# Performance work log

Measured on AMD Instinct MI355X. Metric: run time of the kernel, lower is better.

The kernel has to match this reference:

```python
import jax, jax.numpy as jnp
import numpy as np
import math

H = 1024
N = 64          # d_state; complex modes = N // 2
N2 = N // 2
B = 8
L = 2048
DT_MIN, DT_MAX = 0.001, 0.1


def setup_inputs() -> dict:
    key = jax.random.key(0)
    ks = jax.random.split(key, 8)
    u = jax.random.normal(ks[0], (B, H, L), dtype=jnp.float32)
    # log_dt ~ Uniform[log(dt_min), log(dt_max)]
    log_dt = (jax.random.uniform(ks[1], (H,), dtype=jnp.float32)
              * (math.log(DT_MAX) - math.log(DT_MIN)) + math.log(DT_MIN))
    # random_dplr with scaling='inverse': real part 0.5, imag = (1/pi)*N*(N/(1+2n)-1)
    n = jnp.arange(N2, dtype=jnp.float32)
    w_real = 0.5 * jnp.ones((1, N2), dtype=jnp.float32)
    w_imag = ((1.0 / math.pi) * N * (N / (1.0 + 2.0 * n) - 1.0))[None, :].astype(jnp.float32)
    log_w_real = jnp.log(w_real + 1e-4)  # module stores log(-w.real + 1e-4)
    # C = randn complex (channels=1, H, N2), scaled by normalized B (folded into randn here)
    C_re = jax.random.normal(ks[2], (1, H, N2), dtype=jnp.float32) / math.sqrt(2 * N2)
    C_im = jax.random.normal(ks[3], (1, H, N2), dtype=jnp.float32) / math.sqrt(2 * N2)
    D = jax.random.normal(ks[4], (1, H), dtype=jnp.float32)
    # output_linear: Conv1d(k=1) from channels*H -> H  => weight (H, H)
    W_out = jax.random.normal(ks[5], (H, H), dtype=jnp.float32) / math.sqrt(H)
    b_out = jax.random.normal(ks[6], (H,), dtype=jnp.float32) * 0.01
    return {"u": u, "log_dt": log_dt, "log_w_real": log_w_real, "w_imag": w_imag,
            "C_re": C_re, "C_im": C_im, "D": D, "W_out": W_out, "b_out": b_out}


def reference(u, log_dt, log_w_real, w_imag, C_re, C_im, D, W_out, b_out):
    b, h, l = u.shape
    # --- SSKernelDiag.forward ---
    dt = jnp.exp(log_dt)                                   # (H,)
    w = -jnp.exp(log_w_real) + 1j * w_imag                 # (n_ssm=1, N2)
    w = jnp.broadcast_to(w, (h, w.shape[-1]))              # repeat copies -> (H, N2)
    dtA = w * dt[:, None]                                  # (H, N2) complex
    C = (C_re + 1j * C_im) * (jnp.exp(dtA) - 1.0) / w      # (c, H, N2)
    # Vandermonde: exp(dtA * arange(L)) -> (H, N2, L) complex
    K = jnp.exp(dtA[:, :, None] * jnp.arange(l, dtype=jnp.float32))
    k = 2.0 * jnp.einsum('chn,hnl->chl', C, K).real        # (c, H, L) float
    # --- FFT convolution ---
    k_f = jnp.fft.rfft(k, n=2 * l)                         # (c, H, L+1)
    u_f = jnp.fft.rfft(u, n=2 * l)                         # (B, H, L+1)
    y_f = jnp.einsum('bhl,chl->bchl', u_f, k_f)
    y = jnp.fft.irfft(y_f, n=2 * l)[..., :l]               # (B, c, H, L)
    # skip connection with D
    y = y + jnp.einsum('bhl,ch->bchl', u, D)
    y = y.reshape(b, -1, l)                                # (B, c*H, L)
    y = jax.nn.gelu(y, approximate=False)
    # output 1x1 conv: (B, c*H, L) x (H, c*H) -> (B, H, L)
    y = jnp.einsum('bil,oi->bol', y, W_out) + b_out[None, :, None]
    return y
```

## Files before the change

### kernel.cpp

```cpp
#include <hip/hip_runtime.h>
#include <hip/hip_bf16.h>

#define HH 1024
#define LL 2048
#define BB 8
#define NN2 32
#define CT 128
#define NCH 16

typedef short bf16x8 __attribute__((ext_vector_type(8)));
typedef float f32x4  __attribute__((ext_vector_type(4)));

static __device__ __forceinline__ unsigned short bfbits(float x) {
    __hip_bfloat16 h = __float2bfloat16(x);
    return *(unsigned short*)&h;
}
static __device__ __forceinline__ float f_from_bits(unsigned short b) {
    __hip_bfloat16 h; *(unsigned short*)&h = b; return __bfloat162float(h);
}
static __device__ __forceinline__ float2 cmul(float2 a, float2 b) {
    return make_float2(fmaf(-a.y, b.y, a.x * b.x), fmaf(a.y, b.x, a.x * b.y));
}

#define OFF_U    0
#define OFF_UN   32768
#define OFF_P    49152
#define OFF_KT   65536
#define OFF_DTA  66048
#define OFF_CN   66304
#define OFF_LO   66560
#define OFF_HI   68608
#define LDS_TOT  72960

#define SWZ(off, row) ((off) ^ (((row) & 7) << 4))

__global__ __launch_bounds__(512, 4) void ssm_mfma(
    const float* __restrict__ u, const float* __restrict__ log_dt,
    const float* __restrict__ log_w_real, const float* __restrict__ w_imag,
    const float* __restrict__ C_re, const float* __restrict__ C_im,
    const float* __restrict__ Dp, __hip_bfloat16* __restrict__ g_out)
{
    extern __shared__ char smem[];
    float2* dtA = (float2*)(smem + OFF_DTA);
    float2* Cn  = (float2*)(smem + OFF_CN);
    float*  kt  = (float*)(smem + OFF_KT);
    float2* lo  = (float2*)(smem + OFF_LO);
    float2* hi  = (float2*)(smem + OFF_HI);

    const int tid  = threadIdx.x;
    const int lane = tid & 63;
    const int wave = tid >> 6;
    const int wr4  = wave >> 1;
    const int wc2  = wave & 1;
    const int h    = blockIdx.x;

    float4 ureg[8];
    #pragma unroll
    for (int q = 0; q < 8; ++q) {
        int b = q, c4 = tid;
        ureg[q] = *(const float4*)(u + ((size_t)(b * HH + h)) * LL + c4 * 4);
    }
    if (tid < NN2) {
        int n = tid;
        float dt = expf(log_dt[h]);
        float wr = -expf(log_w_real[n]);
        float wi = w_imag[n];
        float dar = wr * dt, dai = wi * dt;
        dtA[n] = make_float2(dar, dai);
        float er = expf(dar);
        float sn, cs; sincosf(dai, &sn, &cs);
        float exr = er * cs - 1.0f, exi = er * sn;
        float den = wr * wr + wi * wi;
        float fr = (exr * wr + exi * wi) / den;
        float fi = (exi * wr - exr * wi) / den;
        float cre = C_re[h * NN2 + n], cim = C_im[h * NN2 + n];
        Cn[n] = make_float2(cre * fr - cim * fi, cre * fi + cim * fr);
    }
    __syncthreads();

    #pragma unroll
    for (int q = 0; q < 8; ++q) {
        int row = q * 16 + (tid >> 5);
        int j   = (tid & 31) * 4;
        ushort4 o;
        o.x = bfbits(ureg[q].x); o.y = bfbits(ureg[q].y);
        o.z = bfbits(ureg[q].z); o.w = bfbits(ureg[q].w);
        *(ushort4*)(smem + SWZ(OFF_U + row * 256 + j * 2, row)) = o;
    }
    for (int idx = tid; idx < 800; idx += 512) {
        int n, j, p;
        if (idx < 256) { n = idx >> 3; j = idx & 7; p = j; }
        else { int k = idx - 256; n = (k * 241) >> 12; j = k - n * 17; p = j << 3; }
        float2 dA = dtA[n];
        float mag = expf(dA.x * (float)p);
        float sn, cs; sincosf(dA.y * (float)p, &sn, &cs);
        float2 v = make_float2(mag * cs, mag * sn);
        if (idx < 256) lo[n * 8 + j] = v; else hi[n * 17 + j] = v;
    }
    __syncthreads();

    #pragma unroll
    for (int q = 0; q < 2; ++q) {
        int vidx = q * 512 + tid;
        int n = vidx >> 5, j0 = (vidx & 31) * 4;
        float2 a0, a1, a2, a3;
        {
            int p = 127 - j0;       a0 = cmul(lo[n * 8 + (p & 7)], hi[n * 17 + (p >> 3)]);
            p = 126 - j0;           a1 = cmul(lo[n * 8 + (p & 7)], hi[n * 17 + (p >> 3)]);
            p = 125 - j0;           a2 = cmul(lo[n * 8 + (p & 7)], hi[n * 17 + (p >> 3)]);
            p = 124 - j0;           a3 = cmul(lo[n * 8 + (p & 7)], hi[n * 17 + (p >> 3)]);
        }
        ushort4 re, im;
        re.x = bfbits(a0.x); re.y = bfbits(a1.x); re.z = bfbits(a2.x); re.w = bfbits(a3.x);
        im.x = bfbits(a0.y); im.y = bfbits(a1.y); im.z = bfbits(a2.y); im.w = bfbits(a3.y);
        int r0 = 2 * n, r1 = 2 * n + 1;
        *(ushort4*)(smem + SWZ(OFF_UN + r0 * 256 + j0 * 2, r0)) = re;
        *(ushort4*)(smem + SWZ(OFF_UN + r1 * 256 + j0 * 2, r1)) = im;
    }
    {
        int t = tid >> 2, nb = (tid & 3) * 8;
        float s = 0.f;
        #pragma unroll
        for (int i = 0; i < 8; ++i) {
            int n = nb + i;
            float2 a = cmul(lo[n * 8 + (t & 7)], hi[n * 17 + (t >> 3)]);
            float2 C = Cn[n];
            s += C.x * a.x - C.y * a.y;
        }
        s += __shfl_xor(s, 1);
        s += __shfl_xor(s, 2);
        if ((tid & 3) == 0) kt[t] = 2.0f * s;
    }
    __syncthreads();

    f32x4 accP[2][2] = {};
    #pragma unroll
    for (int ks = 0; ks < 4; ++ks) {
        int kf = ks * 32 + (lane >> 4) * 8;
        bf16x8 a0, a1, b0, b1;
        {
            int r = wr4 * 32 + (lane & 15);
            a0 = *(bf16x8*)(smem + SWZ(OFF_U + r * 256 + kf * 2, r));
            int r2 = r + 16;
            a1 = *(bf16x8*)(smem + SWZ(OFF_U + r2 * 256 + kf * 2, r2));
        }
        {
            int r = wc2 * 32 + (lane & 15);
            b0 = *(bf16x8*)(smem + SWZ(OFF_UN + r * 256 + kf * 2, r));
            int r2 = r + 16;
            b1 = *(bf16x8*)(smem + SWZ(OFF_UN + r2 * 256 + kf * 2, r2));
        }
        accP[0][0] = __builtin_amdgcn_mfma_f32_16x16x32_bf16(a0, b0, accP[0][0], 0, 0, 0);
        accP[0][1] = __builtin_amdgcn_mfma_f32_16x16x32_bf16(a0, b1, accP[0][1], 0, 0, 0);
        accP[1][0] = __builtin_amdgcn_mfma_f32_16x16x32_bf16(a1, b0, accP[1][0], 0, 0, 0);
        accP[1][1] = __builtin_amdgcn_mfma_f32_16x16x32_bf16(a1, b1, accP[1][1], 0, 0, 0);
    }
    __syncthreads();
    #pragma unroll
    for (int mt = 0; mt < 2; ++mt)
        #pragma unroll
        for (int nt = 0; nt < 2; ++nt)
            #pragma unroll
            for (int r = 0; r < 4; ++r) {
                int row = wr4 * 32 + mt * 16 + (lane >> 4) * 4 + r;
                int col = wc2 * 32 + nt * 16 + (lane & 15);
                *(unsigned short*)(smem + SWZ(OFF_P + row * 128 + col * 2, row)) =
                    bfbits(accP[mt][nt][r]);
            }
    __syncthreads();

    #pragma unroll
    for (int q = 0; q < 16; ++q) {
        int idx = q * 512 + tid;
        int ttr = idx >> 6, j = idx & 63;
        float val = (ttr >= j) ? kt[ttr - j] : 0.0f;
        *(unsigned short*)(smem + SWZ(OFF_UN + ttr * 128 + j * 2, ttr)) = bfbits(val);
    }
    if (tid < 256) {
        int b = tid >> 5, n = tid & 31;
        float2 C = Cn[n];
        float2 A = hi[n * 17 + 16];
        float sr = 0.f, si = 0.f;
        for (int c = 0; c < NCH; ++c) {
            int row = b * 16 + c;
            int off = SWZ(OFF_P + row * 128 + n * 4, row);
            unsigned int pv = *(unsigned int*)(smem + off);
            float pr = f_from_bits((unsigned short)(pv & 0xffff));
            float pi = f_from_bits((unsigned short)(pv >> 16));
            float csr = C.x * sr - C.y * si;
            float csi = C.x * si + C.y * sr;
            *(unsigned int*)(smem + off) =
                (unsigned)bfbits(csr) | ((unsigned)bfbits(csi) << 16);
            float nsr = A.x * sr - A.y * si + pr;
            float nsi = A.x * si + A.y * sr + pi;
            sr = nsr; si = nsi;
        }
    }
    __syncthreads();

    f32x4 acc[2][4] = {};
    #pragma unroll
    for (int ks = 0; ks < 2; ++ks) {
        int kf = ks * 32 + (lane >> 4) * 8;
        bf16x8 a0, a1, bv[4];
        {
            int r = wr4 * 32 + (lane & 15);
            a0 = *(bf16x8*)(smem + SWZ(OFF_U + r * 256 + kf * 2, r));
            int r2 = r + 16;
            a1 = *(bf16x8*)(smem + SWZ(OFF_U + r2 * 256 + kf * 2, r2));
        }
        #pragma unroll
        for (int nt = 0; nt < 4; ++nt) {
            int ttr = wc2 * 64 + nt * 16 + (lane & 15);
            bv[nt] = *(bf16x8*)(smem + SWZ(OFF_UN + ttr * 128 + kf * 2, ttr));
        }
        #pragma unroll
        for (int nt = 0; nt < 4; ++nt) {
            acc[0][nt] = __builtin_amdgcn_mfma_f32_16x16x32_bf16(a0, bv[nt], acc[0][nt], 0, 0, 0);
            acc[1][nt] = __builtin_amdgcn_mfma_f32_16x16x32_bf16(a1, bv[nt], acc[1][nt], 0, 0, 0);
        }
    }
    __syncthreads();

    #pragma unroll
    for (int q = 0; q < 16; ++q) {
        int idx = q * 512 + tid;
        int ttr = idx >> 6, j = idx & 63;
        float val = (ttr >= 64 + j) ? kt[ttr - 64 - j] : 0.0f;
        *(unsigned short*)(smem + SWZ(OFF_UN + ttr * 128 + j * 2, ttr)) = bfbits(val);
    }
    __syncthreads();
    #pragma unroll
    for (int ks = 0; ks < 2; ++ks) {
        int kf = ks * 32 + (lane >> 4) * 8;
        bf16x8 a0, a1, bv[4];
        {
            int r = wr4 * 32 + (lane & 15);
            a0 = *(bf16x8*)(smem + SWZ(OFF_U + r * 256 + 128 + kf * 2, r));
            int r2 = r + 16;
            a1 = *(bf16x8*)(smem + SWZ(OFF_U + r2 * 256 + 128 + kf * 2, r2));
        }
        #pragma unroll
        for (int nt = 0; nt < 4; ++nt) {
            int ttr = wc2 * 64 + nt * 16 + (lane & 15);
            bv[nt] = *(bf16x8*)(smem + SWZ(OFF_UN + ttr * 128 + kf * 2, ttr));
        }
        #pragma unroll
        for (int nt = 0; nt < 4; ++nt) {
            acc[0][nt] = __builtin_amdgcn_mfma_f32_16x16x32_bf16(a0, bv[nt], acc[0][nt], 0, 0, 0);
            acc[1][nt] = __builtin_amdgcn_mfma_f32_16x16x32_bf16(a1, bv[nt], acc[1][nt], 0, 0, 0);
        }
    }
    __syncthreads();

    #pragma unroll
    for (int q = 0; q < 8; ++q) {
        int idx = q * 512 + tid;
        int n = idx >> 7, ttr = idx & 127;
        int p = ttr + 1;
        float2 a = cmul(lo[n * 8 + (p & 7)], hi[n * 17 + (p >> 3)]);
        int off = SWZ(OFF_UN + ttr * 128 + n * 4, ttr);
        *(unsigned int*)(smem + off) =
            (unsigned)bfbits(2.0f * a.x) | ((unsigned)bfbits(-2.0f * a.y) << 16);
    }
    __syncthreads();
    #pragma unroll
    for (int ks = 0; ks < 2; ++ks) {
        int kf = ks * 32 + (lane >> 4) * 8;
        bf16x8 a0, a1, bv[4];
        {
            int r = wr4 * 32 + (lane & 15);
            a0 = *(bf16x8*)(smem + SWZ(OFF_P + r * 128 + kf * 2, r));
            int r2 = r + 16;
            a1 = *(bf16x8*)(smem + SWZ(OFF_P + r2 * 128 + kf * 2, r2));
        }
        #pragma unroll
        for (int nt = 0; nt < 4; ++nt) {
            int ttr = wc2 * 64 + nt * 16 + (lane & 15);
            bv[nt] = *(bf16x8*)(smem + SWZ(OFF_UN + ttr * 128 + kf * 2, ttr));
        }
        #pragma unroll
        for (int nt = 0; nt < 4; ++nt) {
            acc[0][nt] = __builtin_amdgcn_mfma_f32_16x16x32_bf16(a0, bv[nt], acc[0][nt], 0, 0, 0);
            acc[1][nt] = __builtin_amdgcn_mfma_f32_16x16x32_bf16(a1, bv[nt], acc[1][nt], 0, 0, 0);
        }
    }

    const float Dv = Dp[h];
    #pragma unroll
    for (int mt = 0; mt < 2; ++mt)
        #pragma unroll
        for (int nt = 0; nt < 4; ++nt)
            #pragma unroll
            for (int r = 0; r < 4; ++r) {
                int row = wr4 * 32 + mt * 16 + (lane >> 4) * 4 + r;
                int ttr = wc2 * 64 + nt * 16 + (lane & 15);
                int off = SWZ(OFF_U + row * 256 + ttr * 2, row);
                float uv = f_from_bits(*(unsigned short*)(smem + off));
                float y = acc[mt][nt][r] + Dv * uv;
                float z = 0.7978845608f * (y + 0.044715f * y * y * y);
                float e = __expf(2.0f * z);
                float th = 1.0f - 2.0f / (e + 1.0f);
                float gel = 0.5f * y * (1.0f + th);
                *(unsigned short*)(smem + off) = bfbits(gel);
            }
    __syncthreads();
    #pragma unroll
    for (int q = 0; q < 4; ++q) {
        int flat = q * 512 + tid;
        int row = flat >> 4, c16 = flat & 15;
        uint4 v = *(uint4*)(smem + SWZ(OFF_U + row * 256 + c16 * 16, row));
        int b = row >> 4, c = row & 15;
        *(uint4*)(g_out + ((size_t)(b * HH + h)) * LL + c * CT + c16 * 8) = v;
    }
}

__global__ __launch_bounds__(256) void conv_w(
    const float* __restrict__ W, __hip_bfloat16* __restrict__ Wb)
{
    int i = blockIdx.x * 256 + threadIdx.x;
    float4 v = ((const float4*)W)[i];
    ushort4 o;
    o.x = bfbits(v.x); o.y = bfbits(v.y); o.z = bfbits(v.z); o.w = bfbits(v.w);
    ((ushort4*)Wb)[i] = o;
}

__global__ __launch_bounds__(256) void transpose_g(
    const __hip_bfloat16* __restrict__ g, __hip_bfloat16* __restrict__ gT)
{
    __shared__ __hip_bfloat16 t[64][66];
    const int tid = threadIdx.x;
    const int b  = blockIdx.z;
    const int h0 = blockIdx.x * 64;
    const int l0 = blockIdx.y * 64;

    #pragma unroll
    for (int q = 0; q < 2; ++q) {
        int idx = tid + q * 256;
        int r = idx >> 3, c8 = (idx & 7) * 8;
        uint4 v = *(const uint4*)(g + ((size_t)(b * HH + h0 + r)) * LL + l0 + c8);
        unsigned int* dst = (unsigned int*)&t[r][c8];
        dst[0] = v.x; dst[1] = v.y; dst[2] = v.z; dst[3] = v.w;
    }
    __syncthreads();
    #pragma unroll
    for (int q = 0; q < 2; ++q) {
        int idx = tid + q * 256;
        int r = idx >> 3, c8 = (idx & 7) * 8;
        unsigned short tmp[8];
        #pragma unroll
        for (int j = 0; j < 8; ++j) tmp[j] = *(unsigned short*)&t[c8 + j][r];
        uint4 o;
        o.x = (unsigned)tmp[0] | ((unsigned)tmp[1] << 16);
        o.y = (unsigned)tmp[2] | ((unsigned)tmp[3] << 16);
        o.z = (unsigned)tmp[4] | ((unsigned)tmp[5] << 16);
        o.w = (unsigned)tmp[6] | ((unsigned)tmp[7] << 16);
        *(uint4*)(gT + ((size_t)(b * LL + l0 + r)) * HH + h0 + c8) = o;
    }
}

#define GSLOT 32768
#define STAGE_TILE(kt_, s_)                                                      \
    {                                                                            \
        const int k0_ = (kt_) * 64;                                              \
        _Pragma("unroll")                                                        \
        for (int v_ = 0; v_ < 4; ++v_) {                                         \
            int row_ = v_ * 64 + rsub;                                           \
            const __hip_bfloat16* ga_ = Wb + (size_t)(o0 + row_) * HH + k0_ + csw; \
            const __hip_bfloat16* gb_ = gT + (size_t)(n0 + row_) * HH + k0_ + csw; \
            char* dA_ = smem + (s_) * GSLOT + (v_ * 64 + wave * 8) * 128;        \
            char* dB_ = smem + 2 * GSLOT + (s_) * GSLOT + (v_ * 64 + wave * 8) * 128; \
            __builtin_amdgcn_global_load_lds(                                    \
                (const __attribute__((address_space(1))) void*)ga_,              \
                (__attribute__((address_space(3))) void*)dA_, 16, 0, 0);         \
            __builtin_amdgcn_global_load_lds(                                    \
                (const __attribute__((address_space(1))) void*)gb_,              \
                (__attribute__((address_space(3))) void*)dB_, 16, 0, 0);         \
        }                                                                        \
    }

#define COMPUTE_TILE(s_)                                                         \
    {                                                                            \
        const char* baseA = smem + (s_) * GSLOT;                                 \
        const char* baseB = smem + 2 * GSLOT + (s_) * GSLOT;                     \
        bf16x8 bfr[4][2];                                                        \
        _Pragma("unroll")                                                        \
        for (int nt = 0; nt < 4; ++nt)                                           \
            _Pragma("unroll")                                                    \
            for (int ks = 0; ks < 2; ++ks) {                                     \
                int rb = wn * 64 + nt * 16 + (lane & 15);                        \
                int c  = (ks * 32 + (lane >> 4) * 8) ^ ((rb & 7) << 3);          \
                bfr[nt][ks] = *(const bf16x8*)(baseB + rb * 128 + c * 2);        \
            }                                                                    \
        _Pragma("unroll")                                                        \
        for (int qq = 0; qq < 4; ++qq) {                                         \
            bf16x8 af[2][2];                                                     \
            _Pragma("unroll")                                                    \
            for (int mt = 0; mt < 2; ++mt)                                       \
                _Pragma("unroll")                                                \
                for (int ks = 0; ks < 2; ++ks) {                                 \
                    int ra = wm * 128 + (qq * 2 + mt) * 16 + (lane & 15);        \
                    int c  = (ks * 32 + (lane >> 4) * 8) ^ ((ra & 7) << 3);      \
                    af[mt][ks] = *(const bf16x8*)(baseA + ra * 128 + c * 2);     \
                }                                                                \
            __builtin_amdgcn_s_setprio(1);                                       \
            _Pragma("unroll")                                                    \
            for (int mt = 0; mt < 2; ++mt)                                       \
                _Pragma("unroll")                                                \
                for (int nt = 0; nt < 4; ++nt) {                                 \
                    acc[qq * 2 + mt][nt] = __builtin_amdgcn_mfma_f32_16x16x32_bf16( \
                        af[mt][0], bfr[nt][0], acc[qq * 2 + mt][nt], 0, 0, 0);   \
                    acc[qq * 2 + mt][nt] = __builtin_amdgcn_mfma_f32_16x16x32_bf16( \
                        af[mt][1], bfr[nt][1], acc[qq * 2 + mt][nt], 0, 0, 0);   \
                }                                                                \
            __builtin_amdgcn_s_setprio(0);                                       \
        }                                                                        \
    }

__global__ __launch_bounds__(512, 2) void out_gemm_256(
    const __hip_bfloat16* __restrict__ Wb,
    const __hip_bfloat16* __restrict__ gT,
    const float* __restrict__ bias,
    float* __restrict__ out)
{
    extern __shared__ char smem[];
    const int tid  = threadIdx.x;
    const int lane = tid & 63;
    const int wave = tid >> 6;
    const int wm = wave >> 2;
    const int wn = wave & 3;

    int wg  = blockIdx.x;
    int swz = (wg & 7) * 32 + (wg >> 3);
    const int o0 = (swz & 3) * 256;
    const int n0 = (swz >> 2) * 256;

    const int rsub = tid >> 3;
    const int csw  = ((tid & 7) ^ (rsub & 7)) << 3;

    f32x4 acc[8][4] = {};

    STAGE_TILE(0, 0)
    STAGE_TILE(1, 1)

    for (int t = 0; t < 15; ++t) {
        asm volatile("s_waitcnt vmcnt(8)" ::: "memory");
        __builtin_amdgcn_s_barrier();
        __builtin_amdgcn_sched_barrier(0);
        COMPUTE_TILE(t & 1)
        asm volatile("s_waitcnt lgkmcnt(0)" ::: "memory");
        __builtin_amdgcn_s_barrier();
        __builtin_amdgcn_sched_barrier(0);
        if (t < 14) STAGE_TILE(t + 2, t & 1)
    }
    asm volatile("s_waitcnt vmcnt(0)" ::: "memory");
    __builtin_amdgcn_s_barrier();
    __builtin_amdgcn_sched_barrier(0);
    COMPUTE_TILE(1)

    const int bb = n0 >> 11;
    #pragma unroll
    for (int m = 0; m < 8; ++m) {
        int o = o0 + wm * 128 + m * 16 + (lane >> 4) * 4;
        #pragma unroll
        for (int nt = 0; nt < 4; ++nt) {
            int n = n0 + wn * 64 + nt * 16 + (lane & 15);
            int l = n & 2047;
            #pragma unroll
            for (int r = 0; r < 4; ++r)
                out[((size_t)(bb * HH + o + r)) * LL + l] = acc[m][nt][r] + bias[o + r];
        }
    }
}

extern "C" void kernel_launch(void* const* d_in, const int* in_sizes, int n_in,
                              void* d_out, int out_size, void* d_ws, size_t ws_size,
                              hipStream_t stream) {
    const float* u          = (const float*)d_in[0];
    const float* log_dt     = (const float*)d_in[1];
    const float* log_w_real = (const float*)d_in[2];
    const float* w_imag     = (const float*)d_in[3];
    const float* C_re       = (const float*)d_in[4];
    const float* C_im       = (const float*)d_in[5];
    const float* Dp         = (const float*)d_in[6];
    const float* W          = (const float*)d_in[7];
    const float* bias       = (const float*)d_in[8];
    float* out = (float*)d_out;

    __hip_bfloat16* g  = (__hip_bfloat16*)d_out;
    __hip_bfloat16* gT = (__hip_bfloat16*)d_ws;
    __hip_bfloat16* Wb = (__hip_bfloat16*)((char*)d_ws + 33554432);

    hipFuncSetAttribute((const void*)ssm_mfma,
                        hipFuncAttributeMaxDynamicSharedMemorySize, LDS_TOT);
    hipFuncSetAttribute((const void*)out_gemm_256,
                        hipFuncAttributeMaxDynamicSharedMemorySize, 131072);

    conv_w<<<dim3(HH * HH / 1024), 256, 0, stream>>>(W, Wb);
    ssm_mfma<<<dim3(HH), 512, LDS_TOT, stream>>>(u, log_dt, log_w_real, w_imag,
                                                 C_re, C_im, Dp, g);
    transpose_g<<<dim3(HH / 64, LL / 64, BB), 256, 0, stream>>>(g, gT);
    out_gemm_256<<<dim3(256), 512, 131072, stream>>>(Wb, gT, bias, out);
}
```

Before: 106.9 us.

## Split SSM kernel over batch halves and compute Vandermonde terms directly

Launches the SSM block kernel on a 2D grid, with each block handling four batches instead of eight. This halves LDS use (so launch bounds allow six blocks per CU) and doubles the number of blocks. The lo/hi LDS factor tables for exp(dtA*p) are removed and each term is computed on the fly with fast exp/sin/cos after range reduction. The cost is that the per-head kernel setup (kt, Cn, the Vandermonde build) is now done twice per head, with more transcendental work and lower-precision intrinsics.

```diff
diff --git a/kernel.cpp b/kernel.cpp
--- a/kernel.cpp
+++ b/kernel.cpp
@@ -18,47 +18,48 @@
 static __device__ __forceinline__ float f_from_bits(unsigned short b) {
     __hip_bfloat16 h; *(unsigned short*)&h = b; return __bfloat162float(h);
 }
-static __device__ __forceinline__ float2 cmul(float2 a, float2 b) {
-    return make_float2(fmaf(-a.y, b.y, a.x * b.x), fmaf(a.y, b.x, a.x * b.y));
-}
-
-#define OFF_U    0
-#define OFF_UN   32768
-#define OFF_P    49152
-#define OFF_KT   65536
-#define OFF_DTA  66048
-#define OFF_CN   66304
-#define OFF_LO   66560
-#define OFF_HI   68608
-#define LDS_TOT  72960
+static __device__ __forceinline__ float2 cexp_n(float2 dA, float p) {
+    float mag = __expf(dA.x * p);
+    float rev = dA.y * p * 0.15915494309f;
+    rev -= floorf(rev);
+    float ang = rev * 6.28318530718f;
+    return make_float2(mag * __cosf(ang), mag * __sinf(ang));
+}
+
+#define S_U    0
+#define S_UN   16384
+#define S_P    32768
+#define S_KT   40960
+#define S_DTA  41472
+#define S_CN   41728
+#define S_TOT  41984
 
 #define SWZ(off, row) ((off) ^ (((row) & 7) << 4))
 
-__global__ __launch_bounds__(512, 4) void ssm_mfma(
+__global__ __launch_bounds__(512, 6) void ssm_mfma(
     const float* __restrict__ u, const float* __restrict__ log_dt,
     const float* __restrict__ log_w_real, const float* __restrict__ w_imag,
     const float* __restrict__ C_re, const float* __restrict__ C_im,
     const float* __restrict__ Dp, __hip_bfloat16* __restrict__ g_out)
 {
     extern __shared__ char smem[];
-    float2* dtA = (float2*)(smem + OFF_DTA);
-    float2* Cn  = (float2*)(smem + OFF_CN);
-    float*  kt  = (float*)(smem + OFF_KT);
-    float2* lo  = (float2*)(smem + OFF_LO);
-    float2* hi  = (float2*)(smem + OFF_HI);
+    float2* dtA = (float2*)(smem + S_DTA);
+    float2* Cn  = (float2*)(smem + S_CN);
+    float*  kt  = (float*)(smem + S_KT);
 
     const int tid  = threadIdx.x;
     const int lane = tid & 63;
     const int wave = tid >> 6;
-    const int wr4  = wave >> 1;
-    const int wc2  = wave & 1;
+    const int wm   = wave >> 2;
+    const int wn   = wave & 3;
     const int h    = blockIdx.x;
-
-    float4 ureg[8];
-    #pragma unroll
-    for (int q = 0; q < 8; ++q) {
-        int b = q, c4 = tid;
-        ureg[q] = *(const float4*)(u + ((size_t)(b * HH + h)) * LL + c4 * 4);
+    const int bh   = blockIdx.y;
+
+    float4 ureg[4];
+    #pragma unroll
+    for (int q = 0; q < 4; ++q) {
+        int b = bh * 4 + q;
+        ureg[q] = *(const float4*)(u + ((size_t)(b * HH + h)) * LL + tid * 4);
     }
     if (tid < NN2) {
         int n = tid;
@@ -79,43 +80,29 @@
     __syncthreads();
 
     #pragma unroll
-    for (int q = 0; q < 8; ++q) {
+    for (int q = 0; q < 4; ++q) {
         int row = q * 16 + (tid >> 5);
         int j   = (tid & 31) * 4;
         ushort4 o;
         o.x = bfbits(ureg[q].x); o.y = bfbits(ureg[q].y);
         o.z = bfbits(ureg[q].z); o.w = bfbits(ureg[q].w);
-        *(ushort4*)(smem + SWZ(OFF_U + row * 256 + j * 2, row)) = o;
-    }
-    for (int idx = tid; idx < 800; idx += 512) {
-        int n, j, p;
-        if (idx < 256) { n = idx >> 3; j = idx & 7; p = j; }
-        else { int k = idx - 256; n = (k * 241) >> 12; j = k - n * 17; p = j << 3; }
-        float2 dA = dtA[n];
-        float mag = expf(dA.x * (float)p);
-        float sn, cs; sincosf(dA.y * (float)p, &sn, &cs);
-        float2 v = make_float2(mag * cs, mag * sn);
-        if (idx < 256) lo[n * 8 + j] = v; else hi[n * 17 + j] = v;
-    }
-    __syncthreads();
-
+        *(ushort4*)(smem + SWZ(S_U + row * 256 + j * 2, row)) = o;
+    }
     #pragma unroll
     for (int q = 0; q < 2; ++q) {
         int vidx = q * 512 + tid;
         int n = vidx >> 5, j0 = (vidx & 31) * 4;
-        float2 a0, a1, a2, a3;
-        {
-            int p = 127 - j0;       a0 = cmul(lo[n * 8 + (p & 7)], hi[n * 17 + (p >> 3)]);
-            p = 126 - j0;           a1 = cmul(lo[n * 8 + (p & 7)], hi[n * 17 + (p >> 3)]);
-            p = 125 - j0;           a2 = cmul(lo[n * 8 + (p & 7)], hi[n * 17 + (p >> 3)]);
-            p = 124 - j0;           a3 = cmul(lo[n * 8 + (p & 7)], hi[n * 17 + (p >> 3)]);
-        }
+        float2 dA = dtA[n];
+        float2 a0 = cexp_n(dA, (float)(127 - j0));
+        float2 a1 = cexp_n(dA, (float)(126 - j0));
+        float2 a2 = cexp_n(dA, (float)(125 - j0));
+        float2 a3 = cexp_n(dA, (float)(124 - j0));
         ushort4 re, im;
         re.x = bfbits(a0.x); re.y = bfbits(a1.x); re.z = bfbits(a2.x); re.w = bfbits(a3.x);
         im.x = bfbits(a0.y); im.y = bfbits(a1.y); im.z = bfbits(a2.y); im.w = bfbits(a3.y);
         int r0 = 2 * n, r1 = 2 * n + 1;
-        *(ushort4*)(smem + SWZ(OFF_UN + r0 * 256 + j0 * 2, r0)) = re;
-        *(ushort4*)(smem + SWZ(OFF_UN + r1 * 256 + j0 * 2, r1)) = im;
+        *(ushort4*)(smem + SWZ(S_UN + r0 * 256 + j0 * 2, r0)) = re;
+        *(ushort4*)(smem + SWZ(S_UN + r1 * 256 + j0 * 2, r1)) = im;
     }
     {
         int t = tid >> 2, nb = (tid & 3) * 8;
@@ -123,7 +110,7 @@
         #pragma unroll
         for (int i = 0; i < 8; ++i) {
             int n = nb + i;
-            float2 a = cmul(lo[n * 8 + (t & 7)], hi[n * 17 + (t >> 3)]);
+            float2 a = cexp_n(dtA[n], (float)t);
             float2 C = Cn[n];
             s += C.x * a.x - C.y * a.y;
         }
@@ -133,40 +120,33 @@
     }
     __syncthreads();
 
-    f32x4 accP[2][2] = {};
+    f32x4 accP[2] = {};
     #pragma unroll
     for (int ks = 0; ks < 4; ++ks) {
         int kf = ks * 32 + (lane >> 4) * 8;
-        bf16x8 a0, a1, b0, b1;
+        bf16x8 a0, a1, b0;
         {
-            int r = wr4 * 32 + (lane & 15);
-            a0 = *(bf16x8*)(smem + SWZ(OFF_U + r * 256 + kf * 2, r));
+            int r = wm * 32 + (lane & 15);
+            a0 = *(bf16x8*)(smem + SWZ(S_U + r * 256 + kf * 2, r));
             int r2 = r + 16;
-            a1 = *(bf16x8*)(smem + SWZ(OFF_U + r2 * 256 + kf * 2, r2));
+            a1 = *(bf16x8*)(smem + SWZ(S_U + r2 * 256 + kf * 2, r2));
         }
         {
-            int r = wc2 * 32 + (lane & 15);
-            b0 = *(bf16x8*)(smem + SWZ(OFF_UN + r * 256 + kf * 2, r));
-            int r2 = r + 16;
-            b1 = *(bf16x8*)(smem + SWZ(OFF_UN + r2 * 256 + kf * 2, r2));
-        }
-        accP[0][0] = __builtin_amdgcn_mfma_f32_16x16x32_bf16(a0, b0, accP[0][0], 0, 0, 0);
-        accP[0][1] = __builtin_amdgcn_mfma_f32_16x16x32_bf16(a0, b1, accP[0][1], 0, 0, 0);
-        accP[1][0] = __builtin_amdgcn_mfma_f32_16x16x32_bf16(a1, b0, accP[1][0], 0, 0, 0);
-        accP[1][1] = __builtin_amdgcn_mfma_f32_16x16x32_bf16(a1, b1, accP[1][1], 0, 0, 0);
-    }
-    __syncthreads();
+            int r = wn * 16 + (lane & 15);
+            b0 = *(bf16x8*)(smem + SWZ(S_UN + r * 256 + kf * 2, r));
+        }
+        accP[0] = __builtin_amdgcn_mfma_f32_16x16x32_bf16(a0, b0, accP[0], 0, 0, 0);
+        accP[1] = __builtin_amdgcn_mfma_f32_16x16x32_bf16(a1, b0, accP[1], 0, 0, 0);
+    }
     #pragma unroll
     for (int mt = 0; mt < 2; ++mt)
         #pragma unroll
-        for (int nt = 0; nt < 2; ++nt)
-            #pragma unroll
-            for (int r = 0; r < 4; ++r) {
-                int row = wr4 * 32 + mt * 16 + (lane >> 4) * 4 + r;
-                int col = wc2 * 32 + nt * 16 + (lane & 15);
-                *(unsigned short*)(smem + SWZ(OFF_P + row * 128 + col * 2, row)) =
-                    bfbits(accP[mt][nt][r]);
-            }
+        for (int r = 0; r < 4; ++r) {
+            int row = wm * 32 + mt * 16 + (lane >> 4) * 4 + r;
+            int col = wn * 16 + (lane & 15);
+            *(unsigned short*)(smem + SWZ(S_P + row * 128 + col * 2, row)) =
+                bfbits(accP[mt][r]);
+        }
     __syncthreads();
 
     #pragma unroll
@@ -174,16 +154,16 @@
         int idx = q * 512 + tid;
         int ttr = idx >> 6, j = idx & 63;
         float val = (ttr >= j) ? kt[ttr - j] : 0.0f;
-        *(unsigned short*)(smem + SWZ(OFF_UN + ttr * 128 + j * 2, ttr)) = bfbits(val);
-    }
-    if (tid < 256) {
+        *(unsigned short*)(smem + SWZ(S_UN + ttr * 128 + j * 2, ttr)) = bfbits(val);
+    }
+    if (tid < 128) {
         int b = tid >> 5, n = tid & 31;
         float2 C = Cn[n];
-        float2 A = hi[n * 17 + 16];
+        float2 A = cexp_n(dtA[n], 128.0f);
         float sr = 0.f, si = 0.f;
         for (int c = 0; c < NCH; ++c) {
             int row = b * 16 + c;
-            int off = SWZ(OFF_P + row * 128 + n * 4, row);
+            int off = SWZ(S_P + row * 128 + n * 4, row);
             unsigned int pv = *(unsigned int*)(smem + off);
             float pr = f_from_bits((unsigned short)(pv & 0xffff));
             float pi = f_from_bits((unsigned short)(pv >> 16));
@@ -198,24 +178,24 @@
     }
     __syncthreads();
 
-    f32x4 acc[2][4] = {};
+    f32x4 acc[2][2] = {};
     #pragma unroll
     for (int ks = 0; ks < 2; ++ks) {
         int kf = ks * 32 + (lane >> 4) * 8;
-        bf16x8 a0, a1, bv[4];
+        bf16x8 a0, a1, bv[2];
         {
-            int r = wr4 * 32 + (lane & 15);
-            a0 = *(bf16x8*)(smem + SWZ(OFF_U + r * 256 + kf * 2, r));
+            int r = wm * 32 + (lane & 15);
+            a0 = *(bf16x8*)(smem + SWZ(S_U + r * 256 + kf * 2, r));
             int r2 = r + 16;
-            a1 = *(bf16x8*)(smem + SWZ(OFF_U + r2 * 256 + kf * 2, r2));
-        }
-        #pragma unroll
-        for (int nt = 0; nt < 4; ++nt) {
-            int ttr = wc2 * 64 + nt * 16 + (lane & 15);
-            bv[nt] = *(bf16x8*)(smem + SWZ(OFF_UN + ttr * 128 + kf * 2, ttr));
-        }
-        #pragma unroll
-        for (int nt = 0; nt < 4; ++nt) {
+            a1 = *(bf16x8*)(smem + SWZ(S_U + r2 * 256 + kf * 2, r2));
+        }
+        #pragma unroll
+        for (int nt = 0; nt < 2; ++nt) {
+            int ttr = wn * 32 + nt * 16 + (lane & 15);
+            bv[nt] = *(bf16x8*)(smem + SWZ(S_UN + ttr * 128 + kf * 2, ttr));
+        }
+        #pragma unroll
+        for (int nt = 0; nt < 2; ++nt) {
             acc[0][nt] = __builtin_amdgcn_mfma_f32_16x16x32_bf16(a0, bv[nt], acc[0][nt], 0, 0, 0);
             acc[1][nt] = __builtin_amdgcn_mfma_f32_16x16x32_bf16(a1, bv[nt], acc[1][nt], 0, 0, 0);
         }
@@ -227,26 +207,26 @@
         int idx = q * 512 + tid;
         int ttr = idx >> 6, j = idx & 63;
         float val = (ttr >= 64 + j) ? kt[ttr - 64 - j] : 0.0f;
-        *(unsigned short*)(smem + SWZ(OFF_UN + ttr * 128 + j * 2, ttr)) = bfbits(val);
+        *(unsigned short*)(smem + SWZ(S_UN + ttr * 128 + j * 2, ttr)) = bfbits(val);
     }
     __syncthreads();
     #pragma unroll
     for (int ks = 0; ks < 2; ++ks) {
         int kf = ks * 32 + (lane >> 4) * 8;
-        bf16x8 a0, a1, bv[4];
+        bf16x8 a0, a1, bv[2];
         {
-            int r = wr4 * 32 + (lane & 15);
-            a0 = *(bf16x8*)(smem + SWZ(OFF_U + r * 256 + 128 + kf * 2, r));
+            int r = wm * 32 + (lane & 15);
+            a0 = *(bf16x8*)(smem + SWZ(S_U + r * 256 + 128 + kf * 2, r));
             int r2 = r + 16;
-            a1 = *(bf16x8*)(smem + SWZ(OFF_U + r2 * 256 + 128 + kf * 2, r2));
-        }
-        #pragma unroll
-        for (int nt = 0; nt < 4; ++nt) {
-            int ttr = wc2 * 64 + nt * 16 + (lane & 15);
-            bv[nt] = *(bf16x8*)(smem + SWZ(OFF_UN + ttr * 128 + kf * 2, ttr));
-        }
-        #pragma unroll
-        for (int nt = 0; nt < 4; ++nt) {
+            a1 = *(bf16x8*)(smem + SWZ(S_U + r2 * 256 + 128 + kf * 2, r2));
+        }
+        #pragma unroll
+        for (int nt = 0; nt < 2; ++nt) {
+            int ttr = wn * 32 + nt * 16 + (lane & 15);
+            bv[nt] = *(bf16x8*)(smem + SWZ(S_UN + ttr * 128 + kf * 2, ttr));
+        }
+        #pragma unroll
+        for (int nt = 0; nt < 2; ++nt) {
             acc[0][nt] = __builtin_amdgcn_mfma_f32_16x16x32_bf16(a0, bv[nt], acc[0][nt], 0, 0, 0);
             acc[1][nt] = __builtin_amdgcn_mfma_f32_16x16x32_bf16(a1, bv[nt], acc[1][nt], 0, 0, 0);
         }
@@ -257,9 +237,8 @@
     for (int q = 0; q < 8; ++q) {
         int idx = q * 512 + tid;
         int n = idx >> 7, ttr = idx & 127;
-        int p = ttr + 1;
-        float2 a = cmul(lo[n * 8 + (p & 7)], hi[n * 17 + (p >> 3)]);
-        int off = SWZ(OFF_UN + ttr * 128 + n * 4, ttr);
+        float2 a = cexp_n(dtA[n], (float)(ttr + 1));
+        int off = SWZ(S_UN + ttr * 128 + n * 4, ttr);
         *(unsigned int*)(smem + off) =
             (unsigned)bfbits(2.0f * a.x) | ((unsigned)bfbits(-2.0f * a.y) << 16);
     }
@@ -267,20 +246,20 @@
     #pragma unroll
     for (int ks = 0; ks < 2; ++ks) {
         int kf = ks * 32 + (lane >> 4) * 8;
-        bf16x8 a0, a1, bv[4];
+        bf16x8 a0, a1, bv[2];
         {
-            int r = wr4 * 32 + (lane & 15);
-            a0 = *(bf16x8*)(smem + SWZ(OFF_P + r * 128 + kf * 2, r));
+            int r = wm * 32 + (lane & 15);
+            a0 = *(bf16x8*)(smem + SWZ(S_P + r * 128 + kf * 2, r));
             int r2 = r + 16;
-            a1 = *(bf16x8*)(smem + SWZ(OFF_P + r2 * 128 + kf * 2, r2));
-        }
-        #pragma unroll
-        for (int nt = 0; nt < 4; ++nt) {
-            int ttr = wc2 * 64 + nt * 16 + (lane & 15);
-            bv[nt] = *(bf16x8*)(smem + SWZ(OFF_UN + ttr * 128 + kf * 2, ttr));
-        }
-        #pragma unroll
-        for (int nt = 0; nt < 4; ++nt) {
+            a1 = *(bf16x8*)(smem + SWZ(S_P + r2 * 128 + kf * 2, r2));
+        }
+        #pragma unroll
+        for (int nt = 0; nt < 2; ++nt) {
+            int ttr = wn * 32 + nt * 16 + (lane & 15);
+            bv[nt] = *(bf16x8*)(smem + SWZ(S_UN + ttr * 128 + kf * 2, ttr));
+        }
+        #pragma unroll
+        for (int nt = 0; nt < 2; ++nt) {
             acc[0][nt] = __builtin_amdgcn_mfma_f32_16x16x32_bf16(a0, bv[nt], acc[0][nt], 0, 0, 0);
             acc[1][nt] = __builtin_amdgcn_mfma_f32_16x16x32_bf16(a1, bv[nt], acc[1][nt], 0, 0, 0);
         }
@@ -290,12 +269,12 @@
     #pragma unroll
     for (int mt = 0; mt < 2; ++mt)
         #pragma unroll
-        for (int nt = 0; nt < 4; ++nt)
+        for (int nt = 0; nt < 2; ++nt)
             #pragma unroll
             for (int r = 0; r < 4; ++r) {
-                int row = wr4 * 32 + mt * 16 + (lane >> 4) * 4 + r;
-                int ttr = wc2 * 64 + nt * 16 + (lane & 15);
-                int off = SWZ(OFF_U + row * 256 + ttr * 2, row);
+                int row = wm * 32 + mt * 16 + (lane >> 4) * 4 + r;
+                int ttr = wn * 32 + nt * 16 + (lane & 15);
+                int off = SWZ(S_U + row * 256 + ttr * 2, row);
                 float uv = f_from_bits(*(unsigned short*)(smem + off));
                 float y = acc[mt][nt][r] + Dv * uv;
                 float z = 0.7978845608f * (y + 0.044715f * y * y * y);
@@ -306,11 +285,11 @@
             }
     __syncthreads();
     #pragma unroll
-    for (int q = 0; q < 4; ++q) {
+    for (int q = 0; q < 2; ++q) {
         int flat = q * 512 + tid;
         int row = flat >> 4, c16 = flat & 15;
-        uint4 v = *(uint4*)(smem + SWZ(OFF_U + row * 256 + c16 * 16, row));
-        int b = row >> 4, c = row & 15;
+        uint4 v = *(uint4*)(smem + SWZ(S_U + row * 256 + c16 * 16, row));
+        int b = bh * 4 + (row >> 4), c = row & 15;
         *(uint4*)(g_out + ((size_t)(b * HH + h)) * LL + c * CT + c16 * 8) = v;
     }
 }
@@ -492,13 +471,13 @@
     __hip_bfloat16* Wb = (__hip_bfloat16*)((char*)d_ws + 33554432);
 
     hipFuncSetAttribute((const void*)ssm_mfma,
-                        hipFuncAttributeMaxDynamicSharedMemorySize, LDS_TOT);
+                        hipFuncAttributeMaxDynamicSharedMemorySize, S_TOT);
     hipFuncSetAttribute((const void*)out_gemm_256,
                         hipFuncAttributeMaxDynamicSharedMemorySize, 131072);
 
     conv_w<<<dim3(HH * HH / 1024), 256, 0, stream>>>(W, Wb);
-    ssm_mfma<<<dim3(HH), 512, LDS_TOT, stream>>>(u, log_dt, log_w_real, w_imag,
-                                                 C_re, C_im, Dp, g);
+    ssm_mfma<<<dim3(HH, 2), 512, S_TOT, stream>>>(u, log_dt, log_w_real, w_imag,
+                                                  C_re, C_im, Dp, g);
     transpose_g<<<dim3(HH / 64, LL / 64, BB), 256, 0, stream>>>(g, gT);
     out_gemm_256<<<dim3(256), 512, 131072, stream>>>(Wb, gT, bias, out);
 }
```

Measured after the change: 114.3 us. +6.9%, slower.
